# Performance work log

Hardware: AMD Instinct MI355X
Metric: run time of the kernel (lower is better)

Reference implementation:

```python
import jax, jax.numpy as jnp
import numpy as np

N, E = 50000, 800000
IN_C, OUT_C, H, EW_DIM = 64, 32, 4, 16
NEG_SLOPE = 0.2


def setup_inputs() -> dict:
    key = jax.random.key(0)
    ks = jax.random.split(key, 10)
    x = jax.random.normal(ks[0], (N, IN_C), dtype=jnp.float32)
    src = jax.random.randint(ks[1], (E,), 0, N)
    dst = jax.random.randint(ks[2], (E,), 0, N)
    edge_index = jnp.stack([src, dst]).astype(jnp.int64)
    edge_weight = jax.random.normal(ks[3], (E, EW_DIM), dtype=jnp.float32)
    # GATConv params: lin weight [IN_C, H*OUT_C], bias [H*OUT_C], att_src/att_dst [H, OUT_C]
    s = 1.0 / np.sqrt(IN_C)
    W = jax.random.uniform(ks[4], (IN_C, H * OUT_C), minval=-s, maxval=s, dtype=jnp.float32)
    b = jnp.zeros((H * OUT_C,), dtype=jnp.float32)
    att_src = jax.random.normal(ks[5], (H, OUT_C), dtype=jnp.float32) * 0.1
    att_dst = jax.random.normal(ks[6], (H, OUT_C), dtype=jnp.float32) * 0.1
    # edge_weight_lin params: [EW_DIM, H], [H]
    se = 1.0 / np.sqrt(EW_DIM)
    Wl = jax.random.uniform(ks[7], (EW_DIM, H), minval=-se, maxval=se, dtype=jnp.float32)
    bl = jax.random.uniform(ks[8], (H,), minval=-se, maxval=se, dtype=jnp.float32)
    return {"x": x, "edge_index": edge_index, "edge_weight": edge_weight,
            "W": W, "b": b, "att_src": att_src, "att_dst": att_dst,
            "Wl": Wl, "bl": bl}


def gate_forward(x, edge_index, edge_weight, W, b, att_src, att_dst, Wl, bl):
    n = x.shape[0]
    h = (x @ W).reshape(n, H, OUT_C)                      # [N,H,C]
    a_src = jnp.einsum('nhc,hc->nh', h, att_src)          # [N,H]
    a_dst = jnp.einsum('nhc,hc->nh', h, att_dst)          # [N,H]
    # per-edge attention logits from edge weights (softmax over heads)
    edge_alpha = jax.nn.softmax(edge_weight @ Wl + bl, axis=1)  # [E,H]
    # add self loops (GATConv default add_self_loops=True, fill_value='mean')
    loop = jnp.arange(n)
    src = jnp.concatenate([edge_index[0], loop])
    dst = jnp.concatenate([edge_index[1], loop])
    loop_alpha = jnp.broadcast_to(edge_alpha.mean(axis=0), (n, H))
    ea = jnp.concatenate([edge_alpha, loop_alpha], axis=0)      # [E+N,H]
    # per-edge logits: gather src/dst contributions + edge term
    alpha = jax.nn.leaky_relu(a_src[src] + a_dst[dst] + ea, NEG_SLOPE)  # [E+N,H]
    # segment softmax grouped by destination node
    amax = jax.ops.segment_max(alpha, dst, num_segments=n)
    ex = jnp.exp(alpha - amax[dst])
    denom = jax.ops.segment_sum(ex, dst, num_segments=n)
    alpha = ex / (denom[dst] + 1e-16)                     # [E+N,H]
    # weighted messages, scatter-add aggregate
    msg = h[src] * alpha[:, :, None]                      # [E+N,H,C]
    out = jax.ops.segment_sum(msg, dst, num_segments=n)   # [N,H,C]
    return out.reshape(n, H * OUT_C) + b


def reference(x, edge_index, edge_weight, W, b, att_src, att_dst, Wl, bl):
    return gate_forward(x, edge_index, edge_weight, W, b, att_src, att_dst, Wl, bl)
```

## Files before the change

### kernel.cpp

```cpp
#include <hip/hip_runtime.h>
#include <math.h>

#define IN_C 64
#define HC 128
#define NHEAD 4
#define EWD 16
#define NEG 0.2f

__device__ __forceinline__ float lrelu(float v) { return v > 0.f ? v : NEG * v; }
__device__ __forceinline__ unsigned short f2b(float f) {
    unsigned int u = __float_as_uint(f);
    unsigned int r = ((u >> 16) & 1u) + 0x7fffu;
    return (unsigned short)((u + r) >> 16);
}
__device__ __forceinline__ float b2f(unsigned int lo16) {
    return __uint_as_float(lo16 << 16);
}
__device__ __forceinline__ float pickex(uint4 rec, int head) {
    unsigned int pair = (head & 2) ? rec.z : rec.y;
    unsigned int bits = (head & 1) ? (pair >> 16) : (pair & 0xffffu);
    return b2f(bits);
}

__global__ void __launch_bounds__(128)
k_feat(const float* __restrict__ x, const float* __restrict__ W,
       const float* __restrict__ att_s, const float* __restrict__ att_d,
       unsigned short* __restrict__ h_bf, float* __restrict__ a_src,
       float* __restrict__ a_dst, int N) {
    __shared__ float Ws[IN_C * HC];
    __shared__ float xs[4][IN_C];
    const int tid = threadIdx.x;
    {
        const float4* W4 = (const float4*)W;
        float4* Ws4 = (float4*)Ws;
#pragma unroll
        for (int i = 0; i < 16; ++i)
            Ws4[tid + i * 128] = W4[tid + i * 128];
    }
    const float as = att_s[tid];
    const float ad = att_d[tid];
    const int head = tid >> 5;
    for (int base = blockIdx.x * 4; base < N; base += gridDim.x * 4) {
        const int nrows = min(4, N - base);
        __syncthreads();
        if (tid < 64) {
            int r = tid >> 4, q = tid & 15;
            if (r < nrows)
                ((float4*)&xs[r][0])[q] = ((const float4*)(x + (size_t)(base + r) * IN_C))[q];
        }
        __syncthreads();
        float acc[4] = {0.f, 0.f, 0.f, 0.f};
#pragma unroll
        for (int c = 0; c < IN_C; ++c) {
            const float wv = Ws[c * HC + tid];
#pragma unroll
            for (int r = 0; r < 4; ++r)
                acc[r] = fmaf(xs[r][c], wv, acc[r]);
        }
#pragma unroll
        for (int r = 0; r < 4; ++r) {
            const int n = base + r;
            if (r < nrows) {
                h_bf[(size_t)n * HC + tid] = f2b(acc[r]);
                float ps = acc[r] * as, pd = acc[r] * ad;
#pragma unroll
                for (int off = 16; off; off >>= 1) {
                    ps += __shfl_xor(ps, off, 32);
                    pd += __shfl_xor(pd, off, 32);
                }
                if ((tid & 31) == 0) {
                    a_src[n * NHEAD + head] = ps;
                    a_dst[n * NHEAD + head] = pd;
                }
            }
        }
    }
}

__global__ void k_count(const int* __restrict__ dst, int* __restrict__ deg, int E) {
    const int ebase = blockIdx.x * 1024 + threadIdx.x;
    int d[4];
#pragma unroll
    for (int i = 0; i < 4; ++i) {
        int e = ebase + i * 256;
        d[i] = (e < E) ? dst[e] : -1;
    }
#pragma unroll
    for (int i = 0; i < 4; ++i)
        if (d[i] >= 0) atomicAdd(&deg[d[i]], 1);
}

__global__ void k_scan1(const int* __restrict__ deg, int* __restrict__ part, int N) {
    const int b = blockIdx.x, tid = threadIdx.x;
    int base = b * 1024 + tid * 4;
    int s = 0;
#pragma unroll
    for (int k = 0; k < 4; ++k) { int i = base + k; if (i < N) s += deg[i]; }
#pragma unroll
    for (int off = 32; off; off >>= 1) s += __shfl_xor(s, off, 64);
    __shared__ int ls[4];
    if ((tid & 63) == 0) ls[tid >> 6] = s;
    __syncthreads();
    if (tid == 0) part[b] = ls[0] + ls[1] + ls[2] + ls[3];
}

__global__ void k_scan2(int* part, int nb) {
    const int tid = threadIdx.x;
    int orig = (tid < nb) ? part[tid] : 0;
    int v = orig;
#pragma unroll
    for (int off = 1; off < 64; off <<= 1) {
        int t = __shfl_up(v, off, 64);
        if (tid >= off) v += t;
    }
    if (tid < nb) part[tid] = v - orig;
}

__global__ void k_scan3(const int* __restrict__ deg, const int* __restrict__ part,
                        int* __restrict__ rowptr, int* __restrict__ cursor, int N, int E) {
    const int b = blockIdx.x, tid = threadIdx.x;
    int base = b * 1024 + tid * 4;
    int d[4]; int s = 0;
#pragma unroll
    for (int k = 0; k < 4; ++k) { int i = base + k; d[k] = (i < N) ? deg[i] : 0; s += d[k]; }
    int v = s;
#pragma unroll
    for (int off = 1; off < 64; off <<= 1) {
        int t = __shfl_up(v, off, 64);
        if ((tid & 63) >= off) v += t;
    }
    __shared__ int wsum[4];
    if ((tid & 63) == 63) wsum[tid >> 6] = v;
    __syncthreads();
    int waveoff = 0;
    const int w = tid >> 6;
    for (int k = 0; k < w; ++k) waveoff += wsum[k];
    int excl = v - s + waveoff + part[b];
#pragma unroll
    for (int k = 0; k < 4; ++k) {
        int i = base + k;
        if (i < N) { rowptr[i] = excl; cursor[i] = excl; }
        excl += d[k];
    }
    if (b == 0 && tid == 0) rowptr[N] = E;
}

__global__ void k_fill(const int* __restrict__ src, const int* __restrict__ dst,
                       const float* __restrict__ ew, const float* __restrict__ Wl,
                       const float* __restrict__ bl,
                       const float* __restrict__ a_src, const float* __restrict__ a_dst,
                       int* __restrict__ cursor, uint4* __restrict__ csr,
                       float* __restrict__ partial, int E) {
    __shared__ float sW[EWD * NHEAD];
    __shared__ float sb[NHEAD];
    __shared__ float sred[4][4];
    const int tid = threadIdx.x;
    if (tid < EWD * NHEAD) sW[tid] = Wl[tid];
    if (tid < NHEAD) sb[tid] = bl[tid];
    __syncthreads();
    const int ebase = blockIdx.x * 1024 + tid;
    bool val[4]; int sn[4], dn[4];
#pragma unroll
    for (int i = 0; i < 4; ++i) {
        int e = ebase + i * 256;
        val[i] = e < E;
        int ec = val[i] ? e : 0;
        sn[i] = src[ec];
        dn[i] = dst[ec];
    }
    float4 as4[4], ad4[4];
#pragma unroll
    for (int i = 0; i < 4; ++i) {
        as4[i] = ((const float4*)a_src)[sn[i]];
        ad4[i] = ((const float4*)a_dst)[dn[i]];
    }
    float loc[4] = {0.f, 0.f, 0.f, 0.f};
    unsigned int recy[4], recz[4];
#pragma unroll
    for (int i = 0; i < 4; ++i) {
        int ec = val[i] ? (ebase + i * 256) : 0;
        const float4* w4 = (const float4*)(ew + (size_t)ec * EWD);
        float v[4];
#pragma unroll
        for (int hh = 0; hh < 4; ++hh) v[hh] = sb[hh];
#pragma unroll
        for (int q = 0; q < 4; ++q) {
            float4 t = w4[q];
            float tv[4] = {t.x, t.y, t.z, t.w};
#pragma unroll
            for (int k = 0; k < 4; ++k)
#pragma unroll
                for (int hh = 0; hh < 4; ++hh)
                    v[hh] = fmaf(tv[k], sW[(q * 4 + k) * 4 + hh], v[hh]);
        }
        float m = fmaxf(fmaxf(v[0], v[1]), fmaxf(v[2], v[3]));
        float s = 0.f;
#pragma unroll
        for (int hh = 0; hh < 4; ++hh) { v[hh] = __expf(v[hh] - m); s += v[hh]; }
        float inv = 1.f / s;
#pragma unroll
        for (int hh = 0; hh < 4; ++hh) {
            v[hh] *= inv;
            if (val[i]) loc[hh] += v[hh];
        }
        unsigned int e0 = f2b(__expf(lrelu(as4[i].x + ad4[i].x + v[0])));
        unsigned int e1 = f2b(__expf(lrelu(as4[i].y + ad4[i].y + v[1])));
        unsigned int e2 = f2b(__expf(lrelu(as4[i].z + ad4[i].z + v[2])));
        unsigned int e3 = f2b(__expf(lrelu(as4[i].w + ad4[i].w + v[3])));
        recy[i] = e0 | (e1 << 16);
        recz[i] = e2 | (e3 << 16);
    }
    int slot[4];
#pragma unroll
    for (int i = 0; i < 4; ++i)
        slot[i] = val[i] ? atomicAdd(&cursor[dn[i]], 1) : 0;
#pragma unroll
    for (int i = 0; i < 4; ++i) {
        if (val[i]) {
            uint4 rec;
            rec.x = (unsigned int)sn[i];
            rec.y = recy[i];
            rec.z = recz[i];
            rec.w = 0u;
            csr[slot[i]] = rec;
        }
    }
    const int w = tid >> 6;
#pragma unroll
    for (int hh = 0; hh < 4; ++hh) {
        float v = loc[hh];
#pragma unroll
        for (int off = 32; off; off >>= 1) v += __shfl_xor(v, off, 64);
        if ((tid & 63) == 0) sred[w][hh] = v;
    }
    __syncthreads();
    if (tid < 4)
        partial[blockIdx.x * 4 + tid] =
            sred[0][tid] + sred[1][tid] + sred[2][tid] + sred[3][tid];
}

__global__ void k_red(const float* __restrict__ partial, float* __restrict__ asum, int nb) {
    const int tid = threadIdx.x;
    const int w = tid >> 6, lane = tid & 63;
    float s = 0.f;
    for (int b = lane; b < nb; b += 64) s += partial[b * 4 + w];
#pragma unroll
    for (int off = 32; off; off >>= 1) s += __shfl_xor(s, off, 64);
    if (lane == 0) asum[w] = s;
}

__global__ void k_agg(const unsigned short* __restrict__ h_bf, const int* __restrict__ rowptr,
                      const uint4* __restrict__ csr,
                      const float* __restrict__ a_src, const float* __restrict__ a_dst,
                      const float* __restrict__ asum, const float* __restrict__ bias,
                      float* __restrict__ out, int N, int E) {
    const int d = blockIdx.x;
    const int tid = threadIdx.x;
    const int head = tid >> 5;
    const int r0 = rowptr[d], r1 = rowptr[d + 1];
    float acc = 0.f, den = 0.f;
    int k = r0;
    for (; k + 4 <= r1; k += 4) {
        const uint4 rA = csr[k], rB = csr[k + 1], rC = csr[k + 2], rD = csr[k + 3];
        const float hA = b2f(h_bf[(size_t)rA.x * HC + tid]);
        const float hB = b2f(h_bf[(size_t)rB.x * HC + tid]);
        const float hC = b2f(h_bf[(size_t)rC.x * HC + tid]);
        const float hD = b2f(h_bf[(size_t)rD.x * HC + tid]);
        const float eA = pickex(rA, head), eB = pickex(rB, head);
        const float eC = pickex(rC, head), eD = pickex(rD, head);
        acc = fmaf(hA, eA, acc); den += eA;
        acc = fmaf(hB, eB, acc); den += eB;
        acc = fmaf(hC, eC, acc); den += eC;
        acc = fmaf(hD, eD, acc); den += eD;
    }
    for (; k < r1; ++k) {
        const uint4 rec = csr[k];
        const float hv = b2f(h_bf[(size_t)rec.x * HC + tid]);
        const float ev = pickex(rec, head);
        acc = fmaf(hv, ev, acc); den += ev;
    }
    const float mean = asum[head] * (1.0f / (float)E);
    float l = lrelu(a_src[d * NHEAD + head] + a_dst[d * NHEAD + head] + mean);
    const float exl = __expf(l);
    acc = fmaf(b2f(h_bf[(size_t)d * HC + tid]), exl, acc);
    den += exl;
    out[(size_t)d * HC + tid] = acc / (den + 1e-16f) + bias[tid];
}

extern "C" void kernel_launch(void* const* d_in, const int* in_sizes, int n_in,
                              void* d_out, int out_size, void* d_ws, size_t ws_size,
                              hipStream_t stream) {
    const float* x     = (const float*)d_in[0];
    const int*   ei    = (const int*)d_in[1];
    const float* ew    = (const float*)d_in[2];
    const float* W     = (const float*)d_in[3];
    const float* bias  = (const float*)d_in[4];
    const float* att_s = (const float*)d_in[5];
    const float* att_d = (const float*)d_in[6];
    const float* Wl    = (const float*)d_in[7];
    const float* bl    = (const float*)d_in[8];
    const int N = in_sizes[0] / IN_C;
    const int E = in_sizes[1] / 2;
    const int* src = ei;
    const int* dst = ei + E;
    float* out = (float*)d_out;

    const int FILL_BLOCKS = (E + 1023) / 1024;

    float* ws = (float*)d_ws;
    size_t off = 0;
    unsigned short* h_bf = (unsigned short*)(ws + off); off += (size_t)N * HC / 2;
    float* a_src  = ws + off; off += (size_t)N * NHEAD;
    float* a_dst  = ws + off; off += (size_t)N * NHEAD;
    int*   deg    = (int*)(ws + off); off += N;
    float* asum   = ws + off; off += 4;
    int*   part   = (int*)(ws + off); off += 64;
    int*   rowptr = (int*)(ws + off); off += (size_t)N + 4;
    int*   cursor = (int*)(ws + off); off += N;
    uint4* csr    = (uint4*)(ws + off); off += (size_t)E * 4;
    float* partial= ws + off; off += (size_t)FILL_BLOCKS * 4;

    hipMemsetAsync(deg, 0, (size_t)N * 4, stream);

    k_feat<<<2048, 128, 0, stream>>>(x, W, att_s, att_d, h_bf, a_src, a_dst, N);
    k_count<<<FILL_BLOCKS, 256, 0, stream>>>(dst, deg, E);
    const int nb = (N + 1023) / 1024;
    k_scan1<<<nb, 256, 0, stream>>>(deg, part, N);
    k_scan2<<<1, 64, 0, stream>>>(part, nb);
    k_scan3<<<nb, 256, 0, stream>>>(deg, part, rowptr, cursor, N, E);
    k_fill<<<FILL_BLOCKS, 256, 0, stream>>>(src, dst, ew, Wl, bl, a_src, a_dst,
                                            cursor, csr, partial, E);
    k_red<<<1, 256, 0, stream>>>(partial, asum, FILL_BLOCKS);
    k_agg<<<N, 128, 0, stream>>>(h_bf, rowptr, csr, a_src, a_dst,
                                 asum, bias, out, N, E);
}
```

Measured before the change: 360.7 us.

## Record per-edge slot in count pass, drop cursor atomics in fill, retile feature GEMM

```diff
diff --git a/kernel.cpp b/kernel.cpp
--- a/kernel.cpp
+++ b/kernel.cpp
@@ -28,7 +28,7 @@
        unsigned short* __restrict__ h_bf, float* __restrict__ a_src,
        float* __restrict__ a_dst, int N) {
     __shared__ float Ws[IN_C * HC];
-    __shared__ float xs[4][IN_C];
+    __shared__ float xs[8][IN_C];
     const int tid = threadIdx.x;
     {
         const float4* W4 = (const float4*)W;
@@ -40,25 +40,33 @@
     const float as = att_s[tid];
     const float ad = att_d[tid];
     const int head = tid >> 5;
-    for (int base = blockIdx.x * 4; base < N; base += gridDim.x * 4) {
-        const int nrows = min(4, N - base);
+    for (int base = blockIdx.x * 8; base < N; base += gridDim.x * 8) {
+        const int nrows = min(8, N - base);
         __syncthreads();
-        if (tid < 64) {
+        {
             int r = tid >> 4, q = tid & 15;
             if (r < nrows)
                 ((float4*)&xs[r][0])[q] = ((const float4*)(x + (size_t)(base + r) * IN_C))[q];
         }
         __syncthreads();
-        float acc[4] = {0.f, 0.f, 0.f, 0.f};
-#pragma unroll
-        for (int c = 0; c < IN_C; ++c) {
-            const float wv = Ws[c * HC + tid];
-#pragma unroll
-            for (int r = 0; r < 4; ++r)
-                acc[r] = fmaf(xs[r][c], wv, acc[r]);
+        float acc[8] = {0.f, 0.f, 0.f, 0.f, 0.f, 0.f, 0.f, 0.f};
+#pragma unroll
+        for (int c4 = 0; c4 < IN_C / 4; ++c4) {
+            const float w0 = Ws[(4 * c4 + 0) * HC + tid];
+            const float w1 = Ws[(4 * c4 + 1) * HC + tid];
+            const float w2 = Ws[(4 * c4 + 2) * HC + tid];
+            const float w3 = Ws[(4 * c4 + 3) * HC + tid];
+#pragma unroll
+            for (int r = 0; r < 8; ++r) {
+                const float4 xv = ((const float4*)&xs[r][0])[c4];
+                acc[r] = fmaf(xv.x, w0, acc[r]);
+                acc[r] = fmaf(xv.y, w1, acc[r]);
+                acc[r] = fmaf(xv.z, w2, acc[r]);
+                acc[r] = fmaf(xv.w, w3, acc[r]);
+            }
         }
 #pragma unroll
-        for (int r = 0; r < 4; ++r) {
+        for (int r = 0; r < 8; ++r) {
             const int n = base + r;
             if (r < nrows) {
                 h_bf[(size_t)n * HC + tid] = f2b(acc[r]);
@@ -77,17 +85,10 @@
     }
 }
 
-__global__ void k_count(const int* __restrict__ dst, int* __restrict__ deg, int E) {
-    const int ebase = blockIdx.x * 1024 + threadIdx.x;
-    int d[4];
-#pragma unroll
-    for (int i = 0; i < 4; ++i) {
-        int e = ebase + i * 256;
-        d[i] = (e < E) ? dst[e] : -1;
-    }
-#pragma unroll
-    for (int i = 0; i < 4; ++i)
-        if (d[i] >= 0) atomicAdd(&deg[d[i]], 1);
+__global__ void k_count(const int* __restrict__ dst, int* __restrict__ deg,
+                        int* __restrict__ seq, int E) {
+    int e = blockIdx.x * 256 + threadIdx.x;
+    if (e < E) seq[e] = atomicAdd(&deg[dst[e]], 1);
 }
 
 __global__ void k_scan1(const int* __restrict__ deg, int* __restrict__ part, int N) {
@@ -117,7 +118,7 @@
 }
 
 __global__ void k_scan3(const int* __restrict__ deg, const int* __restrict__ part,
-                        int* __restrict__ rowptr, int* __restrict__ cursor, int N, int E) {
+                        int* __restrict__ rowptr, int N, int E) {
     const int b = blockIdx.x, tid = threadIdx.x;
     int base = b * 1024 + tid * 4;
     int d[4]; int s = 0;
@@ -139,18 +140,18 @@
 #pragma unroll
     for (int k = 0; k < 4; ++k) {
         int i = base + k;
-        if (i < N) { rowptr[i] = excl; cursor[i] = excl; }
+        if (i < N) rowptr[i] = excl;
         excl += d[k];
     }
     if (b == 0 && tid == 0) rowptr[N] = E;
 }
 
 __global__ void k_fill(const int* __restrict__ src, const int* __restrict__ dst,
+                       const int* __restrict__ seq, const int* __restrict__ rowptr,
                        const float* __restrict__ ew, const float* __restrict__ Wl,
                        const float* __restrict__ bl,
                        const float* __restrict__ a_src, const float* __restrict__ a_dst,
-                       int* __restrict__ cursor, uint4* __restrict__ csr,
-                       float* __restrict__ partial, int E) {
+                       uint4* __restrict__ csr, float* __restrict__ partial, int E) {
     __shared__ float sW[EWD * NHEAD];
     __shared__ float sb[NHEAD];
     __shared__ float sred[4][4];
@@ -158,28 +159,15 @@
     if (tid < EWD * NHEAD) sW[tid] = Wl[tid];
     if (tid < NHEAD) sb[tid] = bl[tid];
     __syncthreads();
-    const int ebase = blockIdx.x * 1024 + tid;
-    bool val[4]; int sn[4], dn[4];
-#pragma unroll
-    for (int i = 0; i < 4; ++i) {
-        int e = ebase + i * 256;
-        val[i] = e < E;
-        int ec = val[i] ? e : 0;
-        sn[i] = src[ec];
-        dn[i] = dst[ec];
-    }
-    float4 as4[4], ad4[4];
-#pragma unroll
-    for (int i = 0; i < 4; ++i) {
-        as4[i] = ((const float4*)a_src)[sn[i]];
-        ad4[i] = ((const float4*)a_dst)[dn[i]];
-    }
     float loc[4] = {0.f, 0.f, 0.f, 0.f};
-    unsigned int recy[4], recz[4];
-#pragma unroll
-    for (int i = 0; i < 4; ++i) {
-        int ec = val[i] ? (ebase + i * 256) : 0;
-        const float4* w4 = (const float4*)(ew + (size_t)ec * EWD);
+    const int e = blockIdx.x * 256 + tid;
+    if (e < E) {
+        const int sn = src[e], dn = dst[e];
+        const int sq = seq[e];
+        const int rp = rowptr[dn];
+        float4 as = ((const float4*)a_src)[sn];
+        float4 ad = ((const float4*)a_dst)[dn];
+        const float4* w4 = (const float4*)(ew + (size_t)e * EWD);
         float v[4];
 #pragma unroll
         for (int hh = 0; hh < 4; ++hh) v[hh] = sb[hh];
@@ -199,31 +187,17 @@
         for (int hh = 0; hh < 4; ++hh) { v[hh] = __expf(v[hh] - m); s += v[hh]; }
         float inv = 1.f / s;
 #pragma unroll
-        for (int hh = 0; hh < 4; ++hh) {
-            v[hh] *= inv;
-            if (val[i]) loc[hh] += v[hh];
-        }
-        unsigned int e0 = f2b(__expf(lrelu(as4[i].x + ad4[i].x + v[0])));
-        unsigned int e1 = f2b(__expf(lrelu(as4[i].y + ad4[i].y + v[1])));
-        unsigned int e2 = f2b(__expf(lrelu(as4[i].z + ad4[i].z + v[2])));
-        unsigned int e3 = f2b(__expf(lrelu(as4[i].w + ad4[i].w + v[3])));
-        recy[i] = e0 | (e1 << 16);
-        recz[i] = e2 | (e3 << 16);
-    }
-    int slot[4];
-#pragma unroll
-    for (int i = 0; i < 4; ++i)
-        slot[i] = val[i] ? atomicAdd(&cursor[dn[i]], 1) : 0;
-#pragma unroll
-    for (int i = 0; i < 4; ++i) {
-        if (val[i]) {
-            uint4 rec;
-            rec.x = (unsigned int)sn[i];
-            rec.y = recy[i];
-            rec.z = recz[i];
-            rec.w = 0u;
-            csr[slot[i]] = rec;
-        }
+        for (int hh = 0; hh < 4; ++hh) { v[hh] *= inv; loc[hh] += v[hh]; }
+        unsigned int e0 = f2b(__expf(lrelu(as.x + ad.x + v[0])));
+        unsigned int e1 = f2b(__expf(lrelu(as.y + ad.y + v[1])));
+        unsigned int e2 = f2b(__expf(lrelu(as.z + ad.z + v[2])));
+        unsigned int e3 = f2b(__expf(lrelu(as.w + ad.w + v[3])));
+        uint4 rec;
+        rec.x = (unsigned int)sn;
+        rec.y = e0 | (e1 << 16);
+        rec.z = e2 | (e3 << 16);
+        rec.w = 0u;
+        csr[rp + sq] = rec;
     }
     const int w = tid >> 6;
 #pragma unroll
@@ -305,7 +279,7 @@
     const int* dst = ei + E;
     float* out = (float*)d_out;
 
-    const int FILL_BLOCKS = (E + 1023) / 1024;
+    const int EDGE_BLOCKS = (E + 255) / 256;
 
     float* ws = (float*)d_ws;
     size_t off = 0;
@@ -316,21 +290,21 @@
     float* asum   = ws + off; off += 4;
     int*   part   = (int*)(ws + off); off += 64;
     int*   rowptr = (int*)(ws + off); off += (size_t)N + 4;
-    int*   cursor = (int*)(ws + off); off += N;
+    int*   seq    = (int*)(ws + off); off += E;
     uint4* csr    = (uint4*)(ws + off); off += (size_t)E * 4;
-    float* partial= ws + off; off += (size_t)FILL_BLOCKS * 4;
+    float* partial= ws + off; off += (size_t)EDGE_BLOCKS * 4;
 
     hipMemsetAsync(deg, 0, (size_t)N * 4, stream);
 
     k_feat<<<2048, 128, 0, stream>>>(x, W, att_s, att_d, h_bf, a_src, a_dst, N);
-    k_count<<<FILL_BLOCKS, 256, 0, stream>>>(dst, deg, E);
+    k_count<<<EDGE_BLOCKS, 256, 0, stream>>>(dst, deg, seq, E);
     const int nb = (N + 1023) / 1024;
     k_scan1<<<nb, 256, 0, stream>>>(deg, part, N);
     k_scan2<<<1, 64, 0, stream>>>(part, nb);
-    k_scan3<<<nb, 256, 0, stream>>>(deg, part, rowptr, cursor, N, E);
-    k_fill<<<FILL_BLOCKS, 256, 0, stream>>>(src, dst, ew, Wl, bl, a_src, a_dst,
-                                            cursor, csr, partial, E);
-    k_red<<<1, 256, 0, stream>>>(partial, asum, FILL_BLOCKS);
+    k_scan3<<<nb, 256, 0, stream>>>(deg, part, rowptr, N, E);
+    k_fill<<<EDGE_BLOCKS, 256, 0, stream>>>(src, dst, seq, rowptr, ew, Wl, bl,
+                                            a_src, a_dst, csr, partial, E);
+    k_red<<<1, 256, 0, stream>>>(partial, asum, EDGE_BLOCKS);
     k_agg<<<N, 128, 0, stream>>>(h_bf, rowptr, csr, a_src, a_dst,
                                  asum, bias, out, N, E);
 }
```

New measurement: 386.8 us. 1.07x slower.
